# Optimization experiments

Hardware: AMD Instinct MI355X
Metric: run time of the kernel (lower is better)

## Reference

```python
import jax, jax.numpy as jnp
import numpy as np

BLOCK_DIM = 32
INPUT_DIM = 1024
N_BLOCKS = INPUT_DIM // BLOCK_DIM  # 32
HIDDEN = 2 * BLOCK_DIM             # 64
GAPS = [1, 32]                     # block_dim**i for i in range(num_layers=2)


def setup_inputs() -> dict:
    key = jax.random.key(0)
    ks = jax.random.split(key, 9)
    s = 1.0 / np.sqrt(BLOCK_DIM)
    sh = 1.0 / np.sqrt(HIDDEN)
    return {
        "x": jax.random.normal(ks[0], (16384, INPUT_DIM), dtype=jnp.float32),
        # facto net 0: BlockLinear(32, 32, 64) -> ELU -> BlockLinear(32, 64, 32)
        "W1a": jax.random.uniform(ks[1], (N_BLOCKS, BLOCK_DIM, HIDDEN), jnp.float32, -s, s),
        "b1a": jax.random.uniform(ks[2], (N_BLOCKS, HIDDEN), jnp.float32, -s, s),
        "W2a": jax.random.uniform(ks[3], (N_BLOCKS, HIDDEN, BLOCK_DIM), jnp.float32, -sh, sh),
        "b2a": jax.random.uniform(ks[4], (N_BLOCKS, BLOCK_DIM), jnp.float32, -sh, sh),
        # facto net 1
        "W1b": jax.random.uniform(ks[5], (N_BLOCKS, BLOCK_DIM, HIDDEN), jnp.float32, -s, s),
        "b1b": jax.random.uniform(ks[6], (N_BLOCKS, HIDDEN), jnp.float32, -s, s),
        "W2b": jax.random.uniform(ks[7], (N_BLOCKS, HIDDEN, BLOCK_DIM), jnp.float32, -sh, sh),
        "b2b": jax.random.uniform(ks[8], (N_BLOCKS, BLOCK_DIM), jnp.float32, -sh, sh),
    }


def _block_res_mlp(x, W1, b1, W2, b2):
    # x: (bs, input_dim) -> (n_blocks, bs, block_dim)
    bs = x.shape[0]
    xb = x.reshape(bs, N_BLOCKS, BLOCK_DIM).transpose(1, 0, 2)
    h = jax.nn.elu(jnp.einsum('nbi,nio->nbo', xb, W1) + b1[:, None, :])
    h = jnp.einsum('nbi,nio->nbo', h, W2) + b2[:, None, :]
    yb = h + xb  # residual
    return yb.transpose(1, 0, 2).reshape(bs, -1)


def reference(x, W1a, b1a, W2a, b2a, W1b, b1b, W2b, b2b):
    bs = x.shape[0]
    params = [(W1a, b1a, W2a, b2a), (W1b, b1b, W2b, b2b)]
    y = x
    for gap, (W1, b1, W2, b2) in zip(GAPS, params):
        # strided mixing permutation before the block MLP
        y = y.reshape(-1, BLOCK_DIM, gap).transpose(0, 2, 1).reshape(bs, -1)
        y = _block_res_mlp(y, W1, b1, W2, b2)
        # inverse permutation
        y = y.reshape(-1, gap, BLOCK_DIM).transpose(0, 2, 1)
    return y.reshape(bs, -1)
```

## Files before the change

### kernel.cpp

```cpp
#include <hip/hip_runtime.h>


typedef unsigned short u16t;
typedef __bf16 bf16x8 __attribute__((ext_vector_type(8)));
typedef float f32x4 __attribute__((ext_vector_type(4)));

#define TILE_LD 1032
#define HT_LD   20

__device__ __forceinline__ u16t f2b(float f) {
  union { float f; unsigned u; } v; v.f = f;
  unsigned r = v.u + 0x7FFFu + ((v.u >> 16) & 1u);
  return (u16t)(r >> 16);
}
__device__ __forceinline__ float b2f(u16t h) {
  union { unsigned u; float f; } v; v.u = ((unsigned)h) << 16;
  return v.f;
}

__global__ __launch_bounds__(256) void pack_weights(
    const float* __restrict__ W1a, const float* __restrict__ W2a,
    const float* __restrict__ W1b, const float* __restrict__ W2b,
    u16t* __restrict__ pW1, u16t* __restrict__ pW2) {
  int tidg = blockIdx.x * 256 + threadIdx.x;
  int tensor = tidg >> 14;
  int r  = tidg & 16383;
  int L  = r >> 13;
  int r2 = r & 8191;
  int n    = r2 >> 8;
  int f    = (r2 >> 6) & 3;
  int lane = r2 & 63;
  int q = lane >> 4, t = lane & 15;

  union { u16t us[8]; uint4 v; } w;
  if (tensor == 0) {
    const float* src = L ? W1b : W1a;
#pragma unroll
    for (int j = 0; j < 8; j++)
      w.us[j] = f2b(src[n * 2048 + (q * 8 + j) * 64 + f * 16 + t]);
    *(uint4*)(pW1 + (size_t)((((L * 32 + n) * 4 + f) * 64 + lane) * 8)) = w.v;
  } else {
    const float* src = L ? W2b : W2a;
    int kc = f >> 1, c2 = f & 1;
#pragma unroll
    for (int j = 0; j < 8; j++)
      w.us[j] = f2b(src[n * 2048 + (kc * 32 + q * 8 + j) * 32 + c2 * 16 + t]);
    *(uint4*)(pW2 + (size_t)((((L * 32 + n) * 4 + f) * 64 + lane) * 8)) = w.v;
  }
}

struct Frags {
  bf16x8 w1[4];
  bf16x8 w2[4];
  float  b1v[4];
  float  b2v[2];
};

__device__ __forceinline__ void load_frags(Frags& F, int L, int n, int lane, int t,
    const u16t* __restrict__ pW1, const u16t* __restrict__ pW2,
    const float* __restrict__ b1, const float* __restrict__ b2) {
  const int base = ((L * 32 + n) * 4) * 512 + lane * 8;
#pragma unroll
  for (int f = 0; f < 4; f++) {
    F.w1[f] = *(const bf16x8*)(pW1 + base + f * 512);
    F.w2[f] = *(const bf16x8*)(pW2 + base + f * 512);
  }
#pragma unroll
  for (int c = 0; c < 4; c++) F.b1v[c] = b1[n * 64 + c * 16 + t];
  F.b2v[0] = b2[n * 32 + t];
  F.b2v[1] = b2[n * 32 + 16 + t];
}

template <int L>
__device__ __forceinline__ void compute_layer(
    const bf16x8* afr, u16t* __restrict__ tile, u16t* __restrict__ hT,
    const u16t* __restrict__ pW1, const u16t* __restrict__ pW2,
    const float* __restrict__ b1, const float* __restrict__ b2,
    int wave, int lane, int q, int t, const bf16x8* ifr) {
  const f32x4 zf = {0.f, 0.f, 0.f, 0.f};
  Frags cur, nxt;
  load_frags(cur, L, wave * 8, lane, t, pW1, pW2, b1, b2);
#pragma unroll
  for (int u = 0; u < 8; u++) {
    const int n = wave * 8 + u;
    if (u < 7) load_frags(nxt, L, n + 1, lane, t, pW1, pW2, b1, b2);

    f32x4 accH[4];
#pragma unroll
    for (int c = 0; c < 4; c++)
      accH[c] = __builtin_amdgcn_mfma_f32_16x16x32_bf16(afr[u], cur.w1[c], zf, 0, 0, 0);

#pragma unroll
    for (int c = 0; c < 4; c++) {
      union { u16t us[4]; ushort4 v; } hw;
#pragma unroll
      for (int r = 0; r < 4; r++) {
        float v = accH[c][r] + cur.b1v[c];
        v = v > 0.f ? v : (__expf(v) - 1.f);
        hw.us[r] = f2b(v);
      }
      *(ushort4*)(hT + (c * 16 + t) * HT_LD + 4 * q) = hw.v;
    }

    union { u16t us[8]; bf16x8 v; } a0, a1;
#pragma unroll
    for (int j = 0; j < 8; j++) {
      a0.us[j] = hT[(q * 8 + j) * HT_LD + t];
      a1.us[j] = hT[(32 + q * 8 + j) * HT_LD + t];
    }

#pragma unroll
    for (int c2 = 0; c2 < 2; c2++) {
      f32x4 acc = __builtin_amdgcn_mfma_f32_16x16x32_bf16(afr[u], ifr[c2], zf, 0, 0, 0);
      acc = __builtin_amdgcn_mfma_f32_16x16x32_bf16(a0.v, cur.w2[c2],     acc, 0, 0, 0);
      acc = __builtin_amdgcn_mfma_f32_16x16x32_bf16(a1.v, cur.w2[2 + c2], acc, 0, 0, 0);
#pragma unroll
      for (int r = 0; r < 4; r++) {
        float v = acc[r] + cur.b2v[c2];
        int row = q * 4 + r;
        int cc  = c2 * 16 + t;
        int phys;
        if (L == 0) phys = n * 32 + (cc ^ ((((n >> 3) & 3)) << 1));
        else        phys = (cc * 32 + n) ^ ((cc & 7) << 3);
        tile[row * TILE_LD + phys] = f2b(v);
      }
    }
    cur = nxt;
  }
}

__global__ __launch_bounds__(256) void mixer_kernel(
    const float* __restrict__ x,
    const float* __restrict__ b1a, const float* __restrict__ b2a,
    const float* __restrict__ b1b, const float* __restrict__ b2b,
    const u16t* __restrict__ pW1, const u16t* __restrict__ pW2,
    float* __restrict__ out) {
  __shared__ u16t tile[16 * TILE_LD];
  __shared__ u16t hT[4][64 * HT_LD];

  const int tid  = threadIdx.x;
  const int wave = tid >> 6, lane = tid & 63;
  const int q = lane >> 4, t = lane & 15;
  const int r0 = blockIdx.x * 16;

  bf16x8 ifr[2];
#pragma unroll
  for (int c2 = 0; c2 < 2; c2++) {
    union { u16t us[8]; bf16x8 v; } w;
#pragma unroll
    for (int j = 0; j < 8; j++)
      w.us[j] = ((q * 8 + j) == (c2 * 16 + t)) ? (u16t)0x3F80 : (u16t)0;
    ifr[c2] = w.v;
  }

  bf16x8 afr[8];
#pragma unroll
  for (int u = 0; u < 8; u++) {
    const int n = wave * 8 + u;
    const float* gp = x + (size_t)(r0 + t) * 1024 + n * 32 + q * 8;
    float4 v0 = *(const float4*)gp;
    float4 v1 = *(const float4*)(gp + 4);
    union { u16t us[8]; bf16x8 v; } a;
    a.us[0] = f2b(v0.x); a.us[1] = f2b(v0.y); a.us[2] = f2b(v0.z); a.us[3] = f2b(v0.w);
    a.us[4] = f2b(v1.x); a.us[5] = f2b(v1.y); a.us[6] = f2b(v1.z); a.us[7] = f2b(v1.w);
    afr[u] = a.v;
  }
  compute_layer<0>(afr, tile, hT[wave], pW1, pW2, b1a, b2a, wave, lane, q, t, ifr);
  __syncthreads();

#pragma unroll
  for (int u = 0; u < 8; u++) {
    const int n2 = wave * 8 + u;
    const int nx = n2 ^ (q << 1);
    union { u16t us[8]; bf16x8 v; } a;
#pragma unroll
    for (int j = 0; j < 8; j++)
      a.us[j] = tile[t * TILE_LD + (q * 8 + j) * 32 + nx];
    afr[u] = a.v;
  }
  __syncthreads();
  compute_layer<1>(afr, tile, hT[wave], pW1, pW2, b1b, b2b, wave, lane, q, t, ifr);
  __syncthreads();

#pragma unroll
  for (int i = 0; i < 16; i++) {
    int e = i * 256 + tid;
    int row = e >> 8, g = e & 255;
    int C = 4 * g;
    int phys = C ^ (((g >> 3) & 7) << 3);
    ushort4 hv = *(const ushort4*)(tile + row * TILE_LD + phys);
    float4 o;
    o.x = b2f(hv.x); o.y = b2f(hv.y); o.z = b2f(hv.z); o.w = b2f(hv.w);
    *(float4*)(out + (size_t)(r0 + row) * 1024 + C) = o;
  }
}

extern "C" void kernel_launch(void* const* d_in, const int* in_sizes, int n_in,
                              void* d_out, int out_size, void* d_ws, size_t ws_size,
                              hipStream_t stream) {
  const float* x   = (const float*)d_in[0];
  const float* W1a = (const float*)d_in[1];
  const float* b1a = (const float*)d_in[2];
  const float* W2a = (const float*)d_in[3];
  const float* b2a = (const float*)d_in[4];
  const float* W1b = (const float*)d_in[5];
  const float* b1b = (const float*)d_in[6];
  const float* W2b = (const float*)d_in[7];
  const float* b2b = (const float*)d_in[8];
  float* out = (float*)d_out;

  u16t* pW1 = (u16t*)d_ws;
  u16t* pW2 = pW1 + 131072;

  const int rows = in_sizes[0] / 1024;

  pack_weights<<<128, 256, 0, stream>>>(W1a, W2a, W1b, W2b, pW1, pW2);
  mixer_kernel<<<rows / 16, 256, 0, stream>>>(x, b1a, b2a, b1b, b2b, pW1, pW2, out);
}
```

Before: 157.3 us.

## Transpose MFMA operands to keep hidden activations in registers and swizzle tile

Swaps the A/B operands of the MFMAs so the first GEMM's output layout feeds the second GEMM directly as a register fragment, eliminating the per-wave LDS round-trip for hidden activations. Biases are folded into MFMA accumulator initialisation, ELU becomes branchless, and conversions use hardware bf16 casts. The shared tile drops padding in favour of an XOR swizzle, with launch bounds hinting at 4 blocks per CU. It also drops explicit weight prefetch double-buffering, which may expose global load latency.

```diff
diff --git a/kernel.cpp b/kernel.cpp
--- a/kernel.cpp
+++ b/kernel.cpp
@@ -3,10 +3,8 @@
 
 typedef unsigned short u16t;
 typedef __bf16 bf16x8 __attribute__((ext_vector_type(8)));
+typedef __bf16 bf16x4 __attribute__((ext_vector_type(4)));
 typedef float f32x4 __attribute__((ext_vector_type(4)));
-
-#define TILE_LD 1032
-#define HT_LD   20
 
 __device__ __forceinline__ u16t f2b(float f) {
   union { float f; unsigned u; } v; v.f = f;
@@ -16,6 +14,14 @@
 __device__ __forceinline__ float b2f(u16t h) {
   union { unsigned u; float f; } v; v.u = ((unsigned)h) << 16;
   return v.f;
+}
+__device__ __forceinline__ u16t f2b_hw(float f) {
+  union { __bf16 h; u16t u; } v; v.h = (__bf16)f;
+  return v.u;
+}
+
+__device__ __forceinline__ int swz(int idx) {
+  return idx ^ ((((idx >> 6) ^ (idx >> 10)) & 15) << 2);
 }
 
 __global__ __launch_bounds__(256) void pack_weights(
@@ -41,107 +47,87 @@
     *(uint4*)(pW1 + (size_t)((((L * 32 + n) * 4 + f) * 64 + lane) * 8)) = w.v;
   } else {
     const float* src = L ? W2b : W2a;
-    int kc = f >> 1, c2 = f & 1;
-#pragma unroll
-    for (int j = 0; j < 8; j++)
-      w.us[j] = f2b(src[n * 2048 + (kc * 32 + q * 8 + j) * 32 + c2 * 16 + t]);
+    int e = f >> 1, c2 = f & 1;
+#pragma unroll
+    for (int j = 0; j < 8; j++) {
+      int feat = 32 * e + (j >= 4 ? 16 : 0) + 4 * q + (j & 3);
+      w.us[j] = f2b(src[n * 2048 + feat * 32 + 16 * c2 + t]);
+    }
     *(uint4*)(pW2 + (size_t)((((L * 32 + n) * 4 + f) * 64 + lane) * 8)) = w.v;
   }
-}
-
-struct Frags {
-  bf16x8 w1[4];
-  bf16x8 w2[4];
-  float  b1v[4];
-  float  b2v[2];
-};
-
-__device__ __forceinline__ void load_frags(Frags& F, int L, int n, int lane, int t,
-    const u16t* __restrict__ pW1, const u16t* __restrict__ pW2,
-    const float* __restrict__ b1, const float* __restrict__ b2) {
-  const int base = ((L * 32 + n) * 4) * 512 + lane * 8;
-#pragma unroll
-  for (int f = 0; f < 4; f++) {
-    F.w1[f] = *(const bf16x8*)(pW1 + base + f * 512);
-    F.w2[f] = *(const bf16x8*)(pW2 + base + f * 512);
-  }
-#pragma unroll
-  for (int c = 0; c < 4; c++) F.b1v[c] = b1[n * 64 + c * 16 + t];
-  F.b2v[0] = b2[n * 32 + t];
-  F.b2v[1] = b2[n * 32 + 16 + t];
 }
 
 template <int L>
 __device__ __forceinline__ void compute_layer(
-    const bf16x8* afr, u16t* __restrict__ tile, u16t* __restrict__ hT,
+    const bf16x8* __restrict__ afr, u16t* __restrict__ tile,
     const u16t* __restrict__ pW1, const u16t* __restrict__ pW2,
     const float* __restrict__ b1, const float* __restrict__ b2,
-    int wave, int lane, int q, int t, const bf16x8* ifr) {
-  const f32x4 zf = {0.f, 0.f, 0.f, 0.f};
-  Frags cur, nxt;
-  load_frags(cur, L, wave * 8, lane, t, pW1, pW2, b1, b2);
+    int n0, int lane, int q, int t, const bf16x8* __restrict__ ifr) {
 #pragma unroll
   for (int u = 0; u < 8; u++) {
-    const int n = wave * 8 + u;
-    if (u < 7) load_frags(nxt, L, n + 1, lane, t, pW1, pW2, b1, b2);
-
-    f32x4 accH[4];
+    const int n = n0 + u;
+    const int wbase = ((L * 32 + n) * 4) * 512 + lane * 8;
+
+    bf16x8 w1f[4], w2f[4];
+    f32x4 b1f[4], b2f2[2];
+#pragma unroll
+    for (int c = 0; c < 4; c++) {
+      w1f[c] = *(const bf16x8*)(pW1 + wbase + c * 512);
+      w2f[c] = *(const bf16x8*)(pW2 + wbase + c * 512);
+      b1f[c] = *(const f32x4*)(b1 + n * 64 + c * 16 + q * 4);
+    }
+    b2f2[0] = *(const f32x4*)(b2 + n * 32 + q * 4);
+    b2f2[1] = *(const f32x4*)(b2 + n * 32 + 16 + q * 4);
+
+    f32x4 hacc[4];
 #pragma unroll
     for (int c = 0; c < 4; c++)
-      accH[c] = __builtin_amdgcn_mfma_f32_16x16x32_bf16(afr[u], cur.w1[c], zf, 0, 0, 0);
-
+      hacc[c] = __builtin_amdgcn_mfma_f32_16x16x32_bf16(w1f[c], afr[u], b1f[c], 0, 0, 0);
+
+    bf16x4 av[4];
 #pragma unroll
     for (int c = 0; c < 4; c++) {
-      union { u16t us[4]; ushort4 v; } hw;
 #pragma unroll
       for (int r = 0; r < 4; r++) {
-        float v = accH[c][r] + cur.b1v[c];
-        v = v > 0.f ? v : (__expf(v) - 1.f);
-        hw.us[r] = f2b(v);
+        float v = hacc[c][r];
+        v = fmaxf(v, 0.f) + fminf(__expf(v) - 1.f, 0.f);
+        av[c][r] = (__bf16)v;
       }
-      *(ushort4*)(hT + (c * 16 + t) * HT_LD + 4 * q) = hw.v;
-    }
-
-    union { u16t us[8]; bf16x8 v; } a0, a1;
-#pragma unroll
-    for (int j = 0; j < 8; j++) {
-      a0.us[j] = hT[(q * 8 + j) * HT_LD + t];
-      a1.us[j] = hT[(32 + q * 8 + j) * HT_LD + t];
-    }
+    }
+    bf16x8 bfrag[2];
+#pragma unroll
+    for (int e = 0; e < 2; e++)
+      bfrag[e] = __builtin_shufflevector(av[2 * e], av[2 * e + 1], 0, 1, 2, 3, 4, 5, 6, 7);
 
 #pragma unroll
     for (int c2 = 0; c2 < 2; c2++) {
-      f32x4 acc = __builtin_amdgcn_mfma_f32_16x16x32_bf16(afr[u], ifr[c2], zf, 0, 0, 0);
-      acc = __builtin_amdgcn_mfma_f32_16x16x32_bf16(a0.v, cur.w2[c2],     acc, 0, 0, 0);
-      acc = __builtin_amdgcn_mfma_f32_16x16x32_bf16(a1.v, cur.w2[2 + c2], acc, 0, 0, 0);
+      f32x4 acc = __builtin_amdgcn_mfma_f32_16x16x32_bf16(ifr[c2], afr[u], b2f2[c2], 0, 0, 0);
+#pragma unroll
+      for (int e = 0; e < 2; e++)
+        acc = __builtin_amdgcn_mfma_f32_16x16x32_bf16(w2f[e * 2 + c2], bfrag[e], acc, 0, 0, 0);
 #pragma unroll
       for (int r = 0; r < 4; r++) {
-        float v = acc[r] + cur.b2v[c2];
-        int row = q * 4 + r;
-        int cc  = c2 * 16 + t;
-        int phys;
-        if (L == 0) phys = n * 32 + (cc ^ ((((n >> 3) & 3)) << 1));
-        else        phys = (cc * 32 + n) ^ ((cc & 7) << 3);
-        tile[row * TILE_LD + phys] = f2b(v);
+        int cc  = c2 * 16 + q * 4 + r;
+        int idx = cc * 512 + t * 32 + n;
+        tile[swz(idx)] = f2b_hw(acc[r]);
       }
     }
-    cur = nxt;
-  }
-}
-
-__global__ __launch_bounds__(256) void mixer_kernel(
+  }
+}
+
+__global__ __launch_bounds__(256, 4) void mixer_kernel(
     const float* __restrict__ x,
     const float* __restrict__ b1a, const float* __restrict__ b2a,
     const float* __restrict__ b1b, const float* __restrict__ b2b,
     const u16t* __restrict__ pW1, const u16t* __restrict__ pW2,
     float* __restrict__ out) {
-  __shared__ u16t tile[16 * TILE_LD];
-  __shared__ u16t hT[4][64 * HT_LD];
+  __shared__ u16t tile[16384];
 
   const int tid  = threadIdx.x;
   const int wave = tid >> 6, lane = tid & 63;
   const int q = lane >> 4, t = lane & 15;
   const int r0 = blockIdx.x * 16;
+  const int n0 = wave * 8;
 
   bf16x8 ifr[2];
 #pragma unroll
@@ -156,42 +142,41 @@
   bf16x8 afr[8];
 #pragma unroll
   for (int u = 0; u < 8; u++) {
-    const int n = wave * 8 + u;
-    const float* gp = x + (size_t)(r0 + t) * 1024 + n * 32 + q * 8;
+    const float* gp = x + (size_t)(r0 + t) * 1024 + (n0 + u) * 32 + q * 8;
     float4 v0 = *(const float4*)gp;
     float4 v1 = *(const float4*)(gp + 4);
-    union { u16t us[8]; bf16x8 v; } a;
-    a.us[0] = f2b(v0.x); a.us[1] = f2b(v0.y); a.us[2] = f2b(v0.z); a.us[3] = f2b(v0.w);
-    a.us[4] = f2b(v1.x); a.us[5] = f2b(v1.y); a.us[6] = f2b(v1.z); a.us[7] = f2b(v1.w);
+    union { __bf16 h[8]; bf16x8 v; } a;
+    a.h[0] = (__bf16)v0.x; a.h[1] = (__bf16)v0.y; a.h[2] = (__bf16)v0.z; a.h[3] = (__bf16)v0.w;
+    a.h[4] = (__bf16)v1.x; a.h[5] = (__bf16)v1.y; a.h[6] = (__bf16)v1.z; a.h[7] = (__bf16)v1.w;
     afr[u] = a.v;
   }
-  compute_layer<0>(afr, tile, hT[wave], pW1, pW2, b1a, b2a, wave, lane, q, t, ifr);
+
+  compute_layer<0>(afr, tile, pW1, pW2, b1a, b2a, n0, lane, q, t, ifr);
   __syncthreads();
 
 #pragma unroll
   for (int u = 0; u < 8; u++) {
-    const int n2 = wave * 8 + u;
-    const int nx = n2 ^ (q << 1);
-    union { u16t us[8]; bf16x8 v; } a;
-#pragma unroll
-    for (int j = 0; j < 8; j++)
-      a.us[j] = tile[t * TILE_LD + (q * 8 + j) * 32 + nx];
+    const int n2 = n0 + u;
+    int idx = n2 * 512 + t * 32 + q * 8;
+    union { ushort4 h[2]; bf16x8 v; } a;
+    a.h[0] = *(const ushort4*)&tile[swz(idx)];
+    a.h[1] = *(const ushort4*)&tile[swz(idx + 4)];
     afr[u] = a.v;
   }
   __syncthreads();
-  compute_layer<1>(afr, tile, hT[wave], pW1, pW2, b1b, b2b, wave, lane, q, t, ifr);
+
+  compute_layer<1>(afr, tile, pW1, pW2, b1b, b2b, n0, lane, q, t, ifr);
   __syncthreads();
 
 #pragma unroll
   for (int i = 0; i < 16; i++) {
-    int e = i * 256 + tid;
-    int row = e >> 8, g = e & 255;
-    int C = 4 * g;
-    int phys = C ^ (((g >> 3) & 7) << 3);
-    ushort4 hv = *(const ushort4*)(tile + row * TILE_LD + phys);
+    int c  = tid >> 3;
+    int n2 = (tid & 7) * 4;
+    int idx = c * 512 + i * 32 + n2;
+    ushort4 hv = *(const ushort4*)&tile[swz(idx)];
     float4 o;
     o.x = b2f(hv.x); o.y = b2f(hv.y); o.z = b2f(hv.z); o.w = b2f(hv.w);
-    *(float4*)(out + (size_t)(r0 + row) * 1024 + C) = o;
+    *(float4*)(out + (size_t)(r0 + i) * 1024 + tid * 4) = o;
   }
 }
 
```

New measurement: 198.9 us. 26.4% more time.
